# Kernel optimization log

Measured on AMD Instinct MI355X. Metric: run time of the kernel, lower is better.

The kernel has to match this reference:

```python
import jax, jax.numpy as jnp
import numpy as np

HEAD_SIZE = 64
N_EMBD = 1024
BLOCK_SIZE = 2048


def setup_inputs() -> dict:
    key = jax.random.key(0)
    ks = jax.random.split(key, 7)
    B, T = 4, 2048
    s = 1.0 / np.sqrt(N_EMBD)
    return {
        "x": jax.random.normal(ks[0], (B, T, N_EMBD), dtype=jnp.float32),
        "Wq": jax.random.normal(ks[1], (N_EMBD, HEAD_SIZE), dtype=jnp.float32) * s,
        "bq": jnp.zeros((HEAD_SIZE,), dtype=jnp.float32),
        "Wk": jax.random.normal(ks[2], (N_EMBD, HEAD_SIZE), dtype=jnp.float32) * s,
        "bk": jnp.zeros((HEAD_SIZE,), dtype=jnp.float32),
        "Wv": jax.random.normal(ks[3], (N_EMBD, HEAD_SIZE), dtype=jnp.float32) * s,
        "bv": jnp.zeros((HEAD_SIZE,), dtype=jnp.float32),
    }


def reference(x, Wq, bq, Wk, bk, Wv, bv):
    # x: [B, T, n_embd]
    B, T, _ = x.shape
    q = x @ Wq + bq  # [B, T, H]
    k = x @ Wk + bk
    v = x @ Wv + bv
    # Faithful to source: divides by head_size**(-0.5) == multiplies by sqrt(head_size)
    scale = jnp.float32(HEAD_SIZE) ** 0.5
    scores = jnp.einsum("bqh,bkh->bqk", q, k) * scale  # [B, T, T]
    causal = jnp.tril(jnp.ones((T, T), dtype=bool))
    scores = jnp.where(causal, scores, -jnp.inf)
    attn = jax.nn.softmax(scores, axis=-1)  # dropout p=0.0 (eval)
    out = jnp.einsum("bqk,bkh->bqh", attn, v)  # [B, T, H]
    return out
```

## Files before the change

kernel.cpp:

```cpp
#include <hip/hip_runtime.h>
#include <math.h>

#define NE 1024
#define HS 64
#define TT 2048
#define QSC 11.541560327111707f

typedef __bf16    v8bf __attribute__((ext_vector_type(8)));
typedef _Float16  v8h  __attribute__((ext_vector_type(8)));
typedef float     v4f  __attribute__((ext_vector_type(4)));

#define MFMA_BF(a, b, c)  __builtin_amdgcn_mfma_f32_16x16x32_bf16((a), (b), (c), 0, 0, 0)
#define MFMA_F16(a, b, c) __builtin_amdgcn_mfma_f32_16x16x32_f16((a), (b), (c), 0, 0, 0)

__device__ __forceinline__ void gl_lds16(const void* g, void* l) {
    __builtin_amdgcn_global_load_lds(
        (const __attribute__((address_space(1))) unsigned int*)g,
        (__attribute__((address_space(3))) unsigned int*)l, 16, 0, 0);
}

#define SYNC_VM(imm) do {                                   \
    __asm__ __volatile__("" ::: "memory");                  \
    __builtin_amdgcn_s_waitcnt(imm);                        \
    __builtin_amdgcn_s_barrier();                           \
    __asm__ __volatile__("" ::: "memory");                  \
} while (0)
#define WAIT_VM4  0x0F74
#define WAIT_VM0  0x0F70

__global__ __launch_bounds__(256) void prep_w(
    const float* __restrict__ Wq, const float* __restrict__ Wk,
    const float* __restrict__ Wv, char* __restrict__ imgW)
{
    __shared__ float t[64][65];
    const int bx = blockIdx.x, by = blockIdx.y;
    const float* W = (by == 0) ? Wq : ((by == 1) ? Wk : Wv);
    const int tid = threadIdx.x;
    const int cc = tid & 63, r4 = tid >> 6;
    #pragma unroll
    for (int p = 0; p < 16; ++p) {
        const int k = p * 4 + r4;
        t[k][cc] = W[(size_t)(bx * 64 + k) * HS + cc];
    }
    __syncthreads();
    #pragma unroll
    for (int e = 0; e < 4; ++e) {
        const int chunk = tid + e * 256;
        const int s2   = chunk >> 9;
        const int rem  = chunk & 511;
        const int ctl  = rem >> 7;
        const int rem2 = rem & 127;
        const int pl   = rem2 >> 6;
        const int rem3 = rem2 & 63;
        const int c    = rem3 >> 2;
        const int p16  = rem3 & 3;
        const int kb   = s2 * 32 + ((p16 ^ (c & 3)) << 3);
        const int ncol = ctl * 16 + c;
        v8bf o;
        #pragma unroll
        for (int j = 0; j < 8; ++j) {
            const float v = t[kb + j][ncol];
            const __bf16 h = (__bf16)v;
            o[j] = pl ? (__bf16)(v - (float)h) : h;
        }
        *(v8bf*)(imgW + (size_t)(bx * 2 + s2) * 24576
                 + (by * 4 + ctl) * 2048 + pl * 1024 + c * 64 + p16 * 16) = o;
    }
}

__global__ __launch_bounds__(256, 2) void proj(
    const float* __restrict__ x, const char* __restrict__ imgW,
    const float* __restrict__ bq, const float* __restrict__ bk,
    const float* __restrict__ bv,
    _Float16* __restrict__ qh, _Float16* __restrict__ ql,
    _Float16* __restrict__ kf, _Float16* __restrict__ vt)
{
    __shared__ __align__(16) char sbuf[3][16384];

    const int tid = threadIdx.x, lane = tid & 63, cg = tid >> 6;
    const int quad = lane >> 4, l16 = lane & 15;
    const int bx = blockIdx.x;
    const int m0 = (bx >> 1) * 32;
    const int h  = bx & 1;

    const int xrow = cg * 8 + (lane >> 3);
    const int xp   = (lane >> 1) & 3;
    const int xh   = lane & 1;
    const float* gx = x + (size_t)(m0 + xrow) * NE
                        + ((xp ^ (xrow & 3)) << 3) + (xh << 2);
    const int xl = cg * 1024 + lane * 16;
    const char* gw = imgW + (size_t)h * 12288 + (size_t)tid * 16;

    v4f acc[3];
    #pragma unroll
    for (int i = 0; i < 3; ++i) acc[i] = (v4f){0.f, 0.f, 0.f, 0.f};

    #define STAGE(ks, xb_)  do {                                          \
        gl_lds16(gx + (ks) * 32, (xb_) + xl);                             \
        const char* gws_ = gw + (size_t)(ks) * 24576;                     \
        _Pragma("unroll")                                                 \
        for (int j_ = 0; j_ < 3; ++j_)                                    \
            gl_lds16(gws_ + j_ * 4096, (xb_) + 4096 + tid * 16 + j_ * 4096); \
    } while (0)

    auto compute = [&](int ks) {
        const char* xb = sbuf[ks % 3];
        const char* wb = xb + 4096;
        const int mt = cg >> 1;
        const int wc = cg & 1;
        const int rl = mt * 16 + l16;
        const int pA = quad ^ (rl & 3);
        const float4 a0 = *(const float4*)(xb + rl * 128 + pA * 32);
        const float4 a1 = *(const float4*)(xb + rl * 128 + pA * 32 + 16);
        const float av[8] = {a0.x, a0.y, a0.z, a0.w, a1.x, a1.y, a1.z, a1.w};
        v8bf ah, al;
        #pragma unroll
        for (int i = 0; i < 8; ++i) {
            const __bf16 hv = (__bf16)av[i];
            ah[i] = hv;
            al[i] = (__bf16)(av[i] - (float)hv);
        }
        const int wo = l16 * 64 + ((quad ^ (l16 & 3)) << 4);
        #pragma unroll
        for (int j = 0; j < 3; ++j) {
            const char* base = wb + (wc * 3 + j) * 2048 + wo;
            const v8bf bh = *(const v8bf*)(base);
            const v8bf bl = *(const v8bf*)(base + 1024);
            acc[j] = MFMA_BF(ah, bh, acc[j]);
            acc[j] = MFMA_BF(ah, bl, acc[j]);
            acc[j] = MFMA_BF(al, bh, acc[j]);
        }
    };

    STAGE(0, sbuf[0]);
    STAGE(1, sbuf[1]);
    for (int ks = 0; ks < 31; ++ks) {
        SYNC_VM(WAIT_VM4);
        if (ks + 2 < 32) STAGE(ks + 2, sbuf[(ks + 2) % 3]);
        compute(ks);
    }
    SYNC_VM(WAIT_VM0);
    compute(31);
    #undef STAGE

    const int mt = cg >> 1, wc = cg & 1;
    #pragma unroll
    for (int j = 0; j < 3; ++j) {
        const int n = h * 96 + wc * 48 + j * 16 + l16;
        const float bias = (n < 64) ? bq[n] : ((n < 128) ? bk[n - 64] : bv[n - 128]);
        #pragma unroll
        for (int reg = 0; reg < 4; ++reg) {
            const int row = m0 + mt * 16 + quad * 4 + reg;
            const float v = acc[j][reg] + bias;
            if (n < 64) {
                const float s = v * QSC;
                const _Float16 hh = (_Float16)s;
                qh[(size_t)row * HS + n] = hh;
                ql[(size_t)row * HS + n] = (_Float16)(s - (float)hh);
            } else if (n < 128) {
                kf[(size_t)row * HS + n - 64] = (_Float16)v;
            } else {
                const int b2 = row >> 11, tt = row & 2047, hc = n - 128;
                vt[((size_t)(b2 * HS + hc)) * TT + tt] = (_Float16)v;
            }
        }
    }
}

__global__ __launch_bounds__(512, 2) void attn(
    const _Float16* __restrict__ qh, const _Float16* __restrict__ ql,
    const _Float16* __restrict__ kf, const _Float16* __restrict__ vt,
    float* __restrict__ out)
{
    __shared__ __align__(16) char smem_raw[69632];
    _Float16* ps = (_Float16*)smem_raw;
    float*    os = (float*)smem_raw;
    __shared__ float sm[8][2][16], sl[8][2][16];

    const int tid = threadIdx.x, lane = tid & 63, w = tid >> 6;
    const int quad = lane >> 4, l16 = lane & 15;
    const int b = blockIdx.x & 3, pair = blockIdx.x >> 2;
    const int q0t[2] = {(127 - pair) * 16, pair * 16};
    const int ntk0 = (q0t[0] + 16 + 63) >> 6;
    const int ntk1 = (q0t[1] + 16 + 63) >> 6;
    const int total = ntk0 + ntk1;

    v8h Qh0[2], Qh1[2], Ql0[2], Ql1[2];
    #pragma unroll
    for (int t = 0; t < 2; ++t) {
        const size_t qrow = ((size_t)b * TT + q0t[t] + l16) * HS;
        Qh0[t] = *(const v8h*)(qh + qrow + quad * 8);
        Qh1[t] = *(const v8h*)(qh + qrow + 32 + quad * 8);
        Ql0[t] = *(const v8h*)(ql + qrow + quad * 8);
        Ql1[t] = *(const v8h*)(ql + qrow + 32 + quad * 8);
    }

    const v8h vones = {(_Float16)1.f, (_Float16)1.f, (_Float16)1.f, (_Float16)1.f,
                       (_Float16)1.f, (_Float16)1.f, (_Float16)1.f, (_Float16)1.f};

    float mr0[4] = {-3e38f, -3e38f, -3e38f, -3e38f};
    float mr1[4] = {-3e38f, -3e38f, -3e38f, -3e38f};
    v4f o0[4], o1[4], l40, l41;
    #pragma unroll
    for (int i = 0; i < 4; ++i) {
        o0[i] = (v4f){0.f, 0.f, 0.f, 0.f};
        o1[i] = (v4f){0.f, 0.f, 0.f, 0.f};
    }
    l40 = (v4f){0.f, 0.f, 0.f, 0.f};
    l41 = (v4f){0.f, 0.f, 0.f, 0.f};

    _Float16* pw = ps + w * (16 * 72);

    auto loadK = [&](int j0, v8h (&Kf)[8]) {
        #pragma unroll
        for (int nt = 0; nt < 4; ++nt) {
            const size_t krow = ((size_t)b * TT + j0 + nt * 16 + l16) * HS;
            Kf[nt * 2]     = *(const v8h*)(kf + krow + quad * 8);
            Kf[nt * 2 + 1] = *(const v8h*)(kf + krow + 32 + quad * 8);
        }
    };

    auto doChunk = [&](int j0, int q0c, int t, const v8h (&Kf)[8],
                       float (&mrow)[4], v4f (&o)[4], v4f &o4) {
        v8h Vf[8];
        #pragma unroll
        for (int nt = 0; nt < 4; ++nt) {
            const size_t vrow = ((size_t)(b * HS + nt * 16 + l16)) * TT + j0;
            Vf[nt * 2]     = *(const v8h*)(vt + vrow + quad * 8);
            Vf[nt * 2 + 1] = *(const v8h*)(vt + vrow + 32 + quad * 8);
        }
        v4f s[4];
        #pragma unroll
        for (int i = 0; i < 4; ++i) s[i] = (v4f){0.f, 0.f, 0.f, 0.f};
        #pragma unroll
        for (int nt = 0; nt < 4; ++nt) {
            s[nt] = MFMA_F16(Qh0[t], Kf[nt * 2],     s[nt]);
            s[nt] = MFMA_F16(Qh1[t], Kf[nt * 2 + 1], s[nt]);
            s[nt] = MFMA_F16(Ql0[t], Kf[nt * 2],     s[nt]);
            s[nt] = MFMA_F16(Ql1[t], Kf[nt * 2 + 1], s[nt]);
        }
        const int irow = q0c + quad * 4;
        float mx[4] = {-3e38f, -3e38f, -3e38f, -3e38f};
        #pragma unroll
        for (int nt = 0; nt < 4; ++nt)
            #pragma unroll
            for (int reg = 0; reg < 4; ++reg) {
                if (j0 + nt * 16 + l16 > irow + reg) s[nt][reg] = -3e38f;
                mx[reg] = fmaxf(mx[reg], s[nt][reg]);
            }
        #pragma unroll
        for (int off = 8; off; off >>= 1)
            #pragma unroll
            for (int reg = 0; reg < 4; ++reg)
                mx[reg] = fmaxf(mx[reg], __shfl_xor(mx[reg], off));
        float al[4];
        #pragma unroll
        for (int reg = 0; reg < 4; ++reg) {
            const float mn = fmaxf(mrow[reg], mx[reg]);
            al[reg] = exp2f(mrow[reg] - mn);
            mrow[reg] = mn;
        }
        #pragma unroll
        for (int nt = 0; nt < 4; ++nt)
            #pragma unroll
            for (int reg = 0; reg < 4; ++reg) {
                const float p = (j0 + nt * 16 + l16 > irow + reg)
                                    ? 0.f : exp2f(s[nt][reg] - mrow[reg]);
                pw[(quad * 4 + reg) * 72 + nt * 16 + l16] = (_Float16)p;
            }
        #pragma unroll
        for (int nt = 0; nt < 4; ++nt)
            #pragma unroll
            for (int reg = 0; reg < 4; ++reg)
                o[nt][reg] *= al[reg];
        #pragma unroll
        for (int reg = 0; reg < 4; ++reg)
            o4[reg] *= al[reg];
        const v8h Pa0 = *(const v8h*)(pw + l16 * 72 + quad * 8);
        const v8h Pa1 = *(const v8h*)(pw + l16 * 72 + 32 + quad * 8);
        #pragma unroll
        for (int nt = 0; nt < 4; ++nt) {
            o[nt] = MFMA_F16(Pa0, Vf[nt * 2],     o[nt]);
            o[nt] = MFMA_F16(Pa1, Vf[nt * 2 + 1], o[nt]);
        }
        o4 = MFMA_F16(Pa0, vones, o4);
        o4 = MFMA_F16(Pa1, vones, o4);
    };

    auto jof = [&](int c) { return (c < ntk0) ? c * 64 : (c - ntk0) * 64; };

    {
        v8h KA[8], KB[8];
        int c = w;
        loadK(jof(c), KA);
        while (true) {
            int cn = c + 8;
            if (cn < total) loadK(jof(cn), KB);
            if (c < ntk0) doChunk(c * 64,          q0t[0], 0, KA, mr0, o0, l40);
            else          doChunk((c - ntk0) * 64, q0t[1], 1, KA, mr1, o1, l41);
            if (cn >= total) break;
            c = cn; cn = c + 8;
            if (cn < total) loadK(jof(cn), KA);
            if (c < ntk0) doChunk(c * 64,          q0t[0], 0, KB, mr0, o0, l40);
            else          doChunk((c - ntk0) * 64, q0t[1], 1, KB, mr1, o1, l41);
            if (cn >= total) break;
            c = cn;
        }
    }

    if (l16 == 0) {
        #pragma unroll
        for (int reg = 0; reg < 4; ++reg) {
            sm[w][0][quad * 4 + reg] = mr0[reg];
            sl[w][0][quad * 4 + reg] = l40[reg];
            sm[w][1][quad * 4 + reg] = mr1[reg];
            sl[w][1][quad * 4 + reg] = l41[reg];
        }
    }
    __syncthreads();

    #pragma unroll
    for (int t = 0; t < 2; ++t) {
        float sc[4];
        #pragma unroll
        for (int reg = 0; reg < 4; ++reg) {
            const int r = quad * 4 + reg;
            float M = sm[0][t][r];
            #pragma unroll
            for (int i = 1; i < 8; ++i) M = fmaxf(M, sm[i][t][r]);
            const float mw = t ? mr1[reg] : mr0[reg];
            sc[reg] = exp2f(mw - M);
        }
        float* ow = os + (size_t)(w * 2 + t) * (16 * 68);
        #pragma unroll
        for (int nt = 0; nt < 4; ++nt)
            #pragma unroll
            for (int reg = 0; reg < 4; ++reg) {
                const v4f& oo = t ? o1[nt] : o0[nt];
                ow[(quad * 4 + reg) * 68 + nt * 16 + l16] = oo[reg] * sc[reg];
            }
    }
    __syncthreads();

    #pragma unroll
    for (int kk = 0; kk < 4; ++kk) {
        const int g = w * 4 + kk;
        const int t = g >> 4, m = g & 15;
        float M = sm[0][t][m];
        #pragma unroll
        for (int i = 1; i < 8; ++i) M = fmaxf(M, sm[i][t][m]);
        float L = 0.f, val = 0.f;
        #pragma unroll
        for (int i = 0; i < 8; ++i) {
            L   += sl[i][t][m] * exp2f(sm[i][t][m] - M);
            val += os[(size_t)(i * 2 + t) * (16 * 68) + m * 68 + lane];
        }
        out[((size_t)b * TT + q0t[t] + m) * HS + lane] = val / L;
    }
}

extern "C" void kernel_launch(void* const* d_in, const int* in_sizes, int n_in,
                              void* d_out, int out_size, void* d_ws, size_t ws_size,
                              hipStream_t stream)
{
    const float* x  = (const float*)d_in[0];
    const float* Wq = (const float*)d_in[1];
    const float* bq = (const float*)d_in[2];
    const float* Wk = (const float*)d_in[3];
    const float* bk = (const float*)d_in[4];
    const float* Wv = (const float*)d_in[5];
    const float* bv = (const float*)d_in[6];
    float* out = (float*)d_out;

    const int rows = in_sizes[0] / NE;
    char* p = (char*)d_ws;
    char* imgW = p;                           p += (size_t)32 * 24576;
    _Float16* qhb = (_Float16*)p;             p += (size_t)rows * HS * 2;
    _Float16* qlb = (_Float16*)p;             p += (size_t)rows * HS * 2;
    _Float16* kfb = (_Float16*)p;             p += (size_t)rows * HS * 2;
    _Float16* vtb = (_Float16*)p;             p += (size_t)rows * HS * 2;

    prep_w<<<dim3(16, 3), 256, 0, stream>>>(Wq, Wk, Wv, imgW);
    proj<<<rows / 16, 256, 0, stream>>>(x, imgW, bq, bk, bv,
                                        qhb, qlb, kfb, vtb);
    attn<<<rows / 32, 512, 0, stream>>>(qhb, qlb, kfb, vtb, out);
}
```

Before: 127.8 us.

## Unroll the chunk loop into fixed stages interleaving two KV chunks per wave

```diff
diff --git a/kernel.cpp b/kernel.cpp
--- a/kernel.cpp
+++ b/kernel.cpp
@@ -182,8 +182,6 @@
     const int b = blockIdx.x & 3, pair = blockIdx.x >> 2;
     const int q0t[2] = {(127 - pair) * 16, pair * 16};
     const int ntk0 = (q0t[0] + 16 + 63) >> 6;
-    const int ntk1 = (q0t[1] + 16 + 63) >> 6;
-    const int total = ntk0 + ntk1;
 
     v8h Qh0[2], Qh1[2], Ql0[2], Ql1[2];
     #pragma unroll
@@ -209,7 +207,8 @@
     l40 = (v4f){0.f, 0.f, 0.f, 0.f};
     l41 = (v4f){0.f, 0.f, 0.f, 0.f};
 
-    _Float16* pw = ps + w * (16 * 72);
+    _Float16* pwA = ps + w * 2304;
+    _Float16* pwB = pwA + 1152;
 
     auto loadK = [&](int j0, v8h (&Kf)[8]) {
         #pragma unroll
@@ -219,17 +218,17 @@
             Kf[nt * 2 + 1] = *(const v8h*)(kf + krow + 32 + quad * 8);
         }
     };
-
-    auto doChunk = [&](int j0, int q0c, int t, const v8h (&Kf)[8],
-                       float (&mrow)[4], v4f (&o)[4], v4f &o4) {
-        v8h Vf[8];
+    auto loadV = [&](int j0, v8h (&Vf)[8]) {
         #pragma unroll
         for (int nt = 0; nt < 4; ++nt) {
             const size_t vrow = ((size_t)(b * HS + nt * 16 + l16)) * TT + j0;
             Vf[nt * 2]     = *(const v8h*)(vt + vrow + quad * 8);
             Vf[nt * 2 + 1] = *(const v8h*)(vt + vrow + 32 + quad * 8);
         }
-        v4f s[4];
+    };
+
+    auto qkMask = [&](int j0, int q0c, int t, const v8h (&Kf)[8],
+                      v4f (&s)[4], float (&mx)[4]) {
         #pragma unroll
         for (int i = 0; i < 4; ++i) s[i] = (v4f){0.f, 0.f, 0.f, 0.f};
         #pragma unroll
@@ -240,7 +239,8 @@
             s[nt] = MFMA_F16(Ql1[t], Kf[nt * 2 + 1], s[nt]);
         }
         const int irow = q0c + quad * 4;
-        float mx[4] = {-3e38f, -3e38f, -3e38f, -3e38f};
+        #pragma unroll
+        for (int reg = 0; reg < 4; ++reg) mx[reg] = -3e38f;
         #pragma unroll
         for (int nt = 0; nt < 4; ++nt)
             #pragma unroll
@@ -253,21 +253,29 @@
             #pragma unroll
             for (int reg = 0; reg < 4; ++reg)
                 mx[reg] = fmaxf(mx[reg], __shfl_xor(mx[reg], off));
-        float al[4];
+    };
+
+    auto smStore = [&](int j0, int q0c, const v4f (&s)[4], const float (&mx)[4],
+                       float (&mrow)[4], float (&al)[4], _Float16* pwX) {
         #pragma unroll
         for (int reg = 0; reg < 4; ++reg) {
             const float mn = fmaxf(mrow[reg], mx[reg]);
             al[reg] = exp2f(mrow[reg] - mn);
             mrow[reg] = mn;
         }
+        const int irow = q0c + quad * 4;
         #pragma unroll
         for (int nt = 0; nt < 4; ++nt)
             #pragma unroll
             for (int reg = 0; reg < 4; ++reg) {
                 const float p = (j0 + nt * 16 + l16 > irow + reg)
                                     ? 0.f : exp2f(s[nt][reg] - mrow[reg]);
-                pw[(quad * 4 + reg) * 72 + nt * 16 + l16] = (_Float16)p;
+                pwX[(quad * 4 + reg) * 72 + nt * 16 + l16] = (_Float16)p;
             }
+    };
+
+    auto pvAcc = [&](const float (&al)[4], const v8h (&Vf)[8], _Float16* pwX,
+                     v4f (&o)[4], v4f &o4) {
         #pragma unroll
         for (int nt = 0; nt < 4; ++nt)
             #pragma unroll
@@ -276,8 +284,8 @@
         #pragma unroll
         for (int reg = 0; reg < 4; ++reg)
             o4[reg] *= al[reg];
-        const v8h Pa0 = *(const v8h*)(pw + l16 * 72 + quad * 8);
-        const v8h Pa1 = *(const v8h*)(pw + l16 * 72 + 32 + quad * 8);
+        const v8h Pa0 = *(const v8h*)(pwX + l16 * 72 + quad * 8);
+        const v8h Pa1 = *(const v8h*)(pwX + l16 * 72 + 32 + quad * 8);
         #pragma unroll
         for (int nt = 0; nt < 4; ++nt) {
             o[nt] = MFMA_F16(Pa0, Vf[nt * 2],     o[nt]);
@@ -289,23 +297,47 @@
 
     auto jof = [&](int c) { return (c < ntk0) ? c * 64 : (c - ntk0) * 64; };
 
+    v8h KfA[8], KfB[8], VfA[8], VfB[8];
+    v4f sA[4], sB[4];
+    float mxA[4], mxB[4], alA[4], alB[4];
+
     {
-        v8h KA[8], KB[8];
-        int c = w;
-        loadK(jof(c), KA);
-        while (true) {
-            int cn = c + 8;
-            if (cn < total) loadK(jof(cn), KB);
-            if (c < ntk0) doChunk(c * 64,          q0t[0], 0, KA, mr0, o0, l40);
-            else          doChunk((c - ntk0) * 64, q0t[1], 1, KA, mr1, o1, l41);
-            if (cn >= total) break;
-            c = cn; cn = c + 8;
-            if (cn < total) loadK(jof(cn), KA);
-            if (c < ntk0) doChunk(c * 64,          q0t[0], 0, KB, mr0, o0, l40);
-            else          doChunk((c - ntk0) * 64, q0t[1], 1, KB, mr1, o1, l41);
-            if (cn >= total) break;
-            c = cn;
-        }
+        const int ja = w * 64, jb = (w + 8) * 64;
+        loadK(ja, KfA); loadK(jb, KfB); loadV(ja, VfA);
+        qkMask(ja, q0t[0], 0, KfA, sA, mxA);
+        qkMask(jb, q0t[0], 0, KfB, sB, mxB);
+        loadV(jb, VfB);
+        smStore(ja, q0t[0], sA, mxA, mr0, alA, pwA);
+        smStore(jb, q0t[0], sB, mxB, mr0, alB, pwB);
+        pvAcc(alA, VfA, pwA, o0, l40);
+        pvAcc(alB, VfB, pwB, o0, l40);
+    }
+
+    {
+        const int ca = w + 16, cb = w + 24;
+        const int ja = jof(ca), jb = jof(cb);
+        loadK(ja, KfA); loadK(jb, KfB); loadV(ja, VfA);
+        if (ca < ntk0) qkMask(ja, q0t[0], 0, KfA, sA, mxA);
+        else           qkMask(ja, q0t[1], 1, KfA, sA, mxA);
+        if (cb < ntk0) qkMask(jb, q0t[0], 0, KfB, sB, mxB);
+        else           qkMask(jb, q0t[1], 1, KfB, sB, mxB);
+        loadV(jb, VfB);
+        if (ca < ntk0) smStore(ja, q0t[0], sA, mxA, mr0, alA, pwA);
+        else           smStore(ja, q0t[1], sA, mxA, mr1, alA, pwA);
+        if (cb < ntk0) smStore(jb, q0t[0], sB, mxB, mr0, alB, pwB);
+        else           smStore(jb, q0t[1], sB, mxB, mr1, alB, pwB);
+        if (ca < ntk0) pvAcc(alA, VfA, pwA, o0, l40);
+        else           pvAcc(alA, VfA, pwA, o1, l41);
+        if (cb < ntk0) pvAcc(alB, VfB, pwB, o0, l40);
+        else           pvAcc(alB, VfB, pwB, o1, l41);
+    }
+
+    if (w == 0) {
+        const int j = (32 - ntk0) * 64;
+        loadK(j, KfA); loadV(j, VfA);
+        qkMask(j, q0t[1], 1, KfA, sA, mxA);
+        smStore(j, q0t[1], sA, mxA, mr1, alA, pwA);
+        pvAcc(alA, VfA, pwA, o1, l41);
     }
 
     if (l16 == 0) {
```

New measurement: 128.6 us. Within noise of the previous version (+0.6%).

## Split attention KV range across two blocks and merge partials in a separate kernel

Applied to the files above, without the earlier changes.

```diff
diff --git a/kernel.cpp b/kernel.cpp
--- a/kernel.cpp
+++ b/kernel.cpp
@@ -170,7 +170,7 @@
 __global__ __launch_bounds__(512, 2) void attn(
     const _Float16* __restrict__ qh, const _Float16* __restrict__ ql,
     const _Float16* __restrict__ kf, const _Float16* __restrict__ vt,
-    float* __restrict__ out)
+    float* __restrict__ pM, float* __restrict__ pL, float* __restrict__ pO)
 {
     __shared__ __align__(16) char smem_raw[69632];
     _Float16* ps = (_Float16*)smem_raw;
@@ -179,7 +179,8 @@
 
     const int tid = threadIdx.x, lane = tid & 63, w = tid >> 6;
     const int quad = lane >> 4, l16 = lane & 15;
-    const int b = blockIdx.x & 3, pair = blockIdx.x >> 2;
+    const int bx = blockIdx.x;
+    const int b = bx & 3, half = (bx >> 2) & 1, pair = bx >> 3;
     const int q0t[2] = {(127 - pair) * 16, pair * 16};
     const int ntk0 = (q0t[0] + 16 + 63) >> 6;
     const int ntk1 = (q0t[1] + 16 + 63) >> 6;
@@ -211,18 +212,15 @@
 
     _Float16* pw = ps + w * (16 * 72);
 
-    auto loadK = [&](int j0, v8h (&Kf)[8]) {
+    auto doChunk = [&](int j0, int q0c, int t,
+                       float (&mrow)[4], v4f (&o)[4], v4f &o4) {
+        v8h Kf[8], Vf[8];
         #pragma unroll
         for (int nt = 0; nt < 4; ++nt) {
             const size_t krow = ((size_t)b * TT + j0 + nt * 16 + l16) * HS;
             Kf[nt * 2]     = *(const v8h*)(kf + krow + quad * 8);
             Kf[nt * 2 + 1] = *(const v8h*)(kf + krow + 32 + quad * 8);
         }
-    };
-
-    auto doChunk = [&](int j0, int q0c, int t, const v8h (&Kf)[8],
-                       float (&mrow)[4], v4f (&o)[4], v4f &o4) {
-        v8h Vf[8];
         #pragma unroll
         for (int nt = 0; nt < 4; ++nt) {
             const size_t vrow = ((size_t)(b * HS + nt * 16 + l16)) * TT + j0;
@@ -287,25 +285,9 @@
         o4 = MFMA_F16(Pa1, vones, o4);
     };
 
-    auto jof = [&](int c) { return (c < ntk0) ? c * 64 : (c - ntk0) * 64; };
-
-    {
-        v8h KA[8], KB[8];
-        int c = w;
-        loadK(jof(c), KA);
-        while (true) {
-            int cn = c + 8;
-            if (cn < total) loadK(jof(cn), KB);
-            if (c < ntk0) doChunk(c * 64,          q0t[0], 0, KA, mr0, o0, l40);
-            else          doChunk((c - ntk0) * 64, q0t[1], 1, KA, mr1, o1, l41);
-            if (cn >= total) break;
-            c = cn; cn = c + 8;
-            if (cn < total) loadK(jof(cn), KA);
-            if (c < ntk0) doChunk(c * 64,          q0t[0], 0, KB, mr0, o0, l40);
-            else          doChunk((c - ntk0) * 64, q0t[1], 1, KB, mr1, o1, l41);
-            if (cn >= total) break;
-            c = cn;
-        }
+    for (int c = 2 * w + half; c < total; c += 16) {
+        if (c < ntk0) doChunk(c * 64,          q0t[0], 0, mr0, o0, l40);
+        else          doChunk((c - ntk0) * 64, q0t[1], 1, mr1, o1, l41);
     }
 
     if (l16 == 0) {
@@ -355,8 +337,31 @@
             L   += sl[i][t][m] * exp2f(sm[i][t][m] - M);
             val += os[(size_t)(i * 2 + t) * (16 * 68) + m * 68 + lane];
         }
-        out[((size_t)b * TT + q0t[t] + m) * HS + lane] = val / L;
-    }
+        const int tile = q0t[t] >> 4;
+        const size_t pb = ((size_t)(half * 4 + b) * 128 + tile);
+        pO[pb * 1024 + m * 64 + lane] = val;
+        if (lane == 0) { pM[pb * 16 + m] = M; pL[pb * 16 + m] = L; }
+    }
+}
+
+__global__ __launch_bounds__(256) void merge(
+    const float* __restrict__ pM, const float* __restrict__ pL,
+    const float* __restrict__ pO, float* __restrict__ out)
+{
+    const int gid = blockIdx.x * 256 + threadIdx.x;
+    const int lane = gid & 63;
+    const int r = gid >> 6;
+    const int b = r >> 11, tt = r & 2047;
+    const int tile = tt >> 4, m = tt & 15;
+    const size_t p0 = (size_t)(0 * 4 + b) * 128 + tile;
+    const size_t p1 = (size_t)(1 * 4 + b) * 128 + tile;
+    const float M0 = pM[p0 * 16 + m], M1 = pM[p1 * 16 + m];
+    const float M = fmaxf(M0, M1);
+    const float a0 = exp2f(M0 - M), a1 = exp2f(M1 - M);
+    const float L = pL[p0 * 16 + m] * a0 + pL[p1 * 16 + m] * a1;
+    const float v = pO[p0 * 1024 + m * 64 + lane] * a0
+                  + pO[p1 * 1024 + m * 64 + lane] * a1;
+    out[(size_t)r * HS + lane] = v / L;
 }
 
 extern "C" void kernel_launch(void* const* d_in, const int* in_sizes, int n_in,
@@ -379,9 +384,13 @@
     _Float16* qlb = (_Float16*)p;             p += (size_t)rows * HS * 2;
     _Float16* kfb = (_Float16*)p;             p += (size_t)rows * HS * 2;
     _Float16* vtb = (_Float16*)p;             p += (size_t)rows * HS * 2;
+    float* pM = (float*)p;                    p += (size_t)2 * 4 * 128 * 16 * 4;
+    float* pL = (float*)p;                    p += (size_t)2 * 4 * 128 * 16 * 4;
+    float* pO = (float*)p;                    p += (size_t)2 * 4 * 128 * 16 * 64 * 4;
 
     prep_w<<<dim3(16, 3), 256, 0, stream>>>(Wq, Wk, Wv, imgW);
     proj<<<rows / 16, 256, 0, stream>>>(x, imgW, bq, bk, bv,
                                         qhb, qlb, kfb, vtb);
-    attn<<<rows / 32, 512, 0, stream>>>(qhb, qlb, kfb, vtb, out);
-}
+    attn<<<rows / 16, 512, 0, stream>>>(qhb, qlb, kfb, vtb, pM, pL, pO);
+    merge<<<(rows * HS) / 256, 256, 0, stream>>>(pM, pL, pO, out);
+}
```

New measurement: 139.2 us. +8.9%, slower.
